# Kernel optimization log

Measured on AMD Instinct MI355X. Metric: run time of the kernel, lower is better.

## Reference

```python
import jax, jax.numpy as jnp
import numpy as np

EMBED_DIM = 1024
B, S = 4, 2048
SCALE = float(np.sqrt(EMBED_DIM))


def setup_inputs() -> dict:
    key = jax.random.key(0)
    ks = jax.random.split(key, 9)
    d = EMBED_DIM
    init = 1.0 / np.sqrt(d)
    return {
        "query": jax.random.normal(ks[0], (B, S, d), jnp.float32),
        "key": jax.random.normal(ks[1], (B, S, d), jnp.float32),
        "value": jax.random.normal(ks[2], (B, S, d), jnp.float32),
        "wq": jax.random.uniform(ks[3], (d, d), jnp.float32, -init, init),
        "bq": jax.random.uniform(ks[4], (d,), jnp.float32, -init, init),
        "wk": jax.random.uniform(ks[5], (d, d), jnp.float32, -init, init),
        "bk": jax.random.uniform(ks[6], (d,), jnp.float32, -init, init),
        "wv": jax.random.uniform(ks[7], (d, d), jnp.float32, -init, init),
        "bv": jax.random.uniform(ks[8], (d,), jnp.float32, -init, init),
    }


def reference(query, key, value, wq, bq, wk, bk, wv, bv):
    # Linear projections (torch Linear: x @ W^T + b; here weights stored as [in, out])
    q = query @ wq + bq            # [B,S,D]
    k = key @ wk + bk              # [B,S,D]
    v = value @ wv + bv            # [B,S,D]
    scores = jnp.einsum("bqd,bkd->bqk", q, k) / SCALE   # [B,S,S]
    attn = jax.nn.softmax(scores, axis=-1)
    # dropout in eval mode -> identity
    return jnp.einsum("bqk,bkd->bqd", attn, v)          # [B,S,D]
```

## Files before the change

### kernel.cpp

```cpp
#include <hip/hip_runtime.h>
#include <hip/hip_bf16.h>

typedef __attribute__((ext_vector_type(4))) float   f32x4;
typedef __attribute__((ext_vector_type(8))) __bf16  bf16x8;
typedef __attribute__((ext_vector_type(4))) __bf16  bf16x4;

#define NB 4
#define SS 2048
#define DD 1024

__device__ __forceinline__ void gload_lds16(const void* g, void* l) {
  __builtin_amdgcn_global_load_lds((const __attribute__((address_space(1))) void*)g,
                                   (__attribute__((address_space(3))) void*)l,
                                   16, 0, 0);
}

__global__ __launch_bounds__(256) void cvt_in_kernel(
    const float* __restrict__ q, const float* __restrict__ k,
    const float* __restrict__ v, __bf16* __restrict__ X)
{
  const float* src = blockIdx.z == 0 ? q : (blockIdx.z == 1 ? k : v);
  __bf16* dst = X + (size_t)blockIdx.z * (size_t)(NB * SS * DD);
  size_t i = ((size_t)blockIdx.x * 256 + threadIdx.x) * 4;
  float4 f = *(const float4*)&src[i];
  bf16x4 o = { (__bf16)f.x, (__bf16)f.y, (__bf16)f.z, (__bf16)f.w };
  *(bf16x4*)&dst[i] = o;
}

__global__ __launch_bounds__(256) void prep_w_kernel(
    const float* __restrict__ wq, const float* __restrict__ wk, const float* __restrict__ wv,
    const float* __restrict__ bq, const float* __restrict__ bk, const float* __restrict__ bv,
    __bf16* __restrict__ Wt, float* __restrict__ biasbuf)
{
  const int z = blockIdx.z;
  const float* W  = z == 0 ? wq : (z == 1 ? wk : wv);
  const float* bi = z == 0 ? bq : (z == 1 ? bk : bv);
  __bf16* dst = Wt + (size_t)z * (size_t)(DD * DD);
  const int n0 = blockIdx.x * 32, k0 = blockIdx.y * 32;
  __shared__ float t[32][33];
  const int tx = threadIdx.x & 31, ty = threadIdx.x >> 5;
  #pragma unroll
  for (int i = 0; i < 4; i++)
    t[ty + 8 * i][tx] = W[(size_t)(k0 + ty + 8 * i) * DD + n0 + tx];
  __syncthreads();
  #pragma unroll
  for (int i = 0; i < 4; i++)
    dst[(size_t)(n0 + ty + 8 * i) * DD + k0 + tx] = (__bf16)t[tx][ty + 8 * i];
  if (blockIdx.x == 0 && blockIdx.y == 0) {
    #pragma unroll
    for (int i = 0; i < 4; i++)
      biasbuf[z * DD + threadIdx.x + 256 * i] = bi[threadIdx.x + 256 * i];
  }
}


#define G2A(BUF) ((BUF) * 16384)
#define G2B(BUF) (32768 + (BUF) * 16384)

#define G2_STAGE(BUF, T) do { int t_ = (T); if (t_ >= NT) t_ = 0;               \
  const __bf16* gA_ = Ablk + (size_t)t_ * 64;                                   \
  const __bf16* gB_ = Bblk + (size_t)t_ * 64;                                   \
  gload_lds16(gA_ + o0, smem + G2A(BUF) + tid * 16);                            \
  gload_lds16(gA_ + o1, smem + G2A(BUF) + 4096 + tid * 16);                     \
  gload_lds16(gA_ + o2, smem + G2A(BUF) + 8192 + tid * 16);                     \
  gload_lds16(gA_ + o3, smem + G2A(BUF) + 12288 + tid * 16);                    \
  gload_lds16(gB_ + o0, smem + G2B(BUF) + tid * 16);                            \
  gload_lds16(gB_ + o1, smem + G2B(BUF) + 4096 + tid * 16);                     \
  gload_lds16(gB_ + o2, smem + G2B(BUF) + 8192 + tid * 16);                     \
  gload_lds16(gB_ + o3, smem + G2B(BUF) + 12288 + tid * 16); } while (0)

template <int EPI>
__global__ __launch_bounds__(256, 2) void gemm2b_kernel(
    const __bf16* __restrict__ A, const __bf16* __restrict__ B,
    const float* __restrict__ bias, float* __restrict__ Fout,
    __bf16* __restrict__ Qo, __bf16* __restrict__ Ko, __bf16* __restrict__ Vt,
    int K, int lda, int ldb, int ldc,
    long strideA, long strideB, long strideC)
{
  extern __shared__ char smem[];

  const int gx = gridDim.x, gy = gridDim.y;
  const int nwg = gx * gy * gridDim.z;
  int lin = blockIdx.x + gx * (blockIdx.y + gy * blockIdx.z);
  const int cpx = nwg >> 3;
  int swz = (lin & 7) * cpx + (lin >> 3);
  const int bx = swz % gx;
  int rem = swz / gx;
  const int by = rem % gy;
  const int bz = rem / gy;

  const long brow = (long)by * 128, bcol = (long)bx * 128;
  const __bf16* Ablk = A + (size_t)bz * strideA + (size_t)brow * lda;
  const __bf16* Bblk = B + (size_t)bz * strideB + (size_t)bcol * ldb;

  const int tid  = threadIdx.x;
  const int lane = tid & 63;
  const int wid  = tid >> 6;
  const int wm = wid >> 1, wn = wid & 1;
  const int l15 = lane & 15, l4 = lane >> 4;
  const int lx = (lane & 7) << 4;

  const int NT = K >> 6;

  int o0, o1, o2, o3;
  #pragma unroll
  for (int i = 0; i < 4; ++i) {
    const int p = i * 4096 + tid * 16;
    const int r = p >> 7;
    const int kb = (p ^ ((r & 7) << 4)) & 127;
    const int off = r * lda + (kb >> 1);
    if (i == 0) o0 = off; else if (i == 1) o1 = off;
    else if (i == 2) o2 = off; else o3 = off;
  }

  int ara[2], brb[2];
  #pragma unroll
  for (int ks = 0; ks < 2; ++ks) {
    ara[ks] = ((((wm * 64 + l15) * 64 + l4 * 8) * 2) + ks * 64) ^ lx;
    brb[ks] = ((((wn * 64 + l15) * 64 + l4 * 8) * 2) + ks * 64) ^ lx;
  }

  f32x4 acc[4][4] = {};
  f32x4 accs[4] = {};
  bf16x8 af[4][2], bf[4][2];
  bf16x8 onesf;
  #pragma unroll
  for (int j = 0; j < 8; ++j) onesf[j] = (__bf16)1.0f;

  G2_STAGE(0, 0);
  G2_STAGE(1, 1);
  asm volatile("s_waitcnt vmcnt(8)" ::: "memory");
  __builtin_amdgcn_s_barrier();

  for (int t = 0; t < NT; ++t) {
    const int cur = t & 1;
    const int abase = cur * 16384;
    const int bbase = 32768 + cur * 16384;
    #pragma unroll
    for (int mi = 0; mi < 4; ++mi)
      #pragma unroll
      for (int ks = 0; ks < 2; ++ks)
        af[mi][ks] = *(const bf16x8*)(smem + abase + ara[ks] + mi * 2048);
    #pragma unroll
    for (int ni = 0; ni < 4; ++ni)
      #pragma unroll
      for (int ks = 0; ks < 2; ++ks)
        bf[ni][ks] = *(const bf16x8*)(smem + bbase + brb[ks] + ni * 2048);
    asm volatile("s_waitcnt lgkmcnt(0)" ::: "memory");
    __builtin_amdgcn_sched_barrier(0);
    __builtin_amdgcn_s_barrier();
    G2_STAGE(cur, t + 2);
    __builtin_amdgcn_s_setprio(1);
    #pragma unroll
    for (int mi = 0; mi < 4; ++mi)
      #pragma unroll
      for (int ni = 0; ni < 4; ++ni)
        #pragma unroll
        for (int ks = 0; ks < 2; ++ks)
          acc[mi][ni] = __builtin_amdgcn_mfma_f32_16x16x32_bf16(
              af[mi][ks], bf[ni][ks], acc[mi][ni], 0, 0, 0);
    if constexpr (EPI == 2) {
      #pragma unroll
      for (int mi = 0; mi < 4; ++mi)
        #pragma unroll
        for (int ks = 0; ks < 2; ++ks)
          accs[mi] = __builtin_amdgcn_mfma_f32_16x16x32_bf16(
              af[mi][ks], onesf, accs[mi], 0, 0, 0);
    }
    __builtin_amdgcn_s_setprio(0);
    __builtin_amdgcn_sched_barrier(0);
    asm volatile("s_waitcnt vmcnt(8)" ::: "memory");
    __builtin_amdgcn_s_barrier();
  }

  if constexpr (EPI == 2) {
    float* C = Fout + (size_t)bz * strideC;
    #pragma unroll
    for (int mi = 0; mi < 4; ++mi) {
      f32x4 inv;
      #pragma unroll
      for (int e = 0; e < 4; ++e) inv[e] = 1.0f / accs[mi][e];
      #pragma unroll
      for (int ni = 0; ni < 4; ++ni) {
        const long row = brow + wm * 64 + mi * 16 + l4 * 4;
        const long col = bcol + wn * 64 + ni * 16 + l15;
        #pragma unroll
        for (int e = 0; e < 4; ++e)
          C[(row + e) * (size_t)ldc + col] = acc[mi][ni][e] * inv[e];
      }
    }
  } else {
    if (bz == 2) {
      #pragma unroll
      for (int mi = 0; mi < 4; ++mi) {
        #pragma unroll
        for (int ni = 0; ni < 4; ++ni) {
          const long row = brow + wm * 64 + mi * 16 + l4 * 4;
          const long col = bcol + wn * 64 + ni * 16 + l15;
          const float bvv = bias[2 * DD + col];
          const long bb = row >> 11, s = row & 2047;
          bf16x4 pk = { (__bf16)(acc[mi][ni][0] + bvv), (__bf16)(acc[mi][ni][1] + bvv),
                        (__bf16)(acc[mi][ni][2] + bvv), (__bf16)(acc[mi][ni][3] + bvv) };
          *(bf16x4*)&Vt[bb * 2097152 + col * 2048 + s] = pk;
        }
      }
    } else {
      __bf16* C = bz == 0 ? Qo : Ko;
      #pragma unroll
      for (int mi = 0; mi < 4; ++mi) {
        #pragma unroll
        for (int ni = 0; ni < 4; ++ni) {
          const long row = brow + wm * 64 + mi * 16 + l4 * 4;
          const long col = bcol + wn * 64 + ni * 16 + l15;
          const float bvv = bias[bz * DD + col];
          #pragma unroll
          for (int e = 0; e < 4; ++e)
            C[(row + e) * 1024 + col] = (__bf16)(acc[mi][ni][e] + bvv);
        }
      }
    }
  }
}


#define A_OFF(BUF, MH) (((BUF)*2 + (MH)) * 16384)
#define B_OFF(BUF, NH) (65536 + ((BUF)*2 + (NH)) * 16384)

#define STAGE_A(BUF, MH, T) do { int t_ = (T); if (t_ >= NT) t_ = 0;            \
  const __bf16* gs_ = Ablk + (size_t)(MH) * (64 * (size_t)lda) + (size_t)t_ * 64; \
  gload_lds16(gs_ + aoff0, smem + A_OFF(BUF, MH) + tid * 16);                    \
  gload_lds16(gs_ + aoff1, smem + A_OFF(BUF, MH) + 8192 + tid * 16); } while (0)

#define STAGE_B(BUF, NH, T) do { int t_ = (T); if (t_ >= NT) t_ = 0;            \
  const __bf16* gs_ = Bblk + (size_t)(NH) * (32 * (size_t)ldb) + (size_t)t_ * 64; \
  gload_lds16(gs_ + boff0, smem + B_OFF(BUF, NH) + tid * 16);                    \
  gload_lds16(gs_ + boff1, smem + B_OFF(BUF, NH) + 8192 + tid * 16); } while (0)

#define DSREAD_A(DST, BUF, MH)                                                  \
  _Pragma("unroll") for (int mi = 0; mi < 4; ++mi) {                            \
    _Pragma("unroll") for (int ks = 0; ks < 2; ++ks)                            \
      DST[mi][ks] = *(const bf16x8*)(smem + A_OFF(BUF, MH) + arb[ks] + mi * 2048); }

#define DSREAD_BS(DST, BUF, NH)                                                 \
  _Pragma("unroll") for (int ni = 0; ni < 2; ++ni) {                            \
    _Pragma("unroll") for (int ks = 0; ks < 2; ++ks)                            \
      DST[ni][ks] = *(const bf16x8*)(smem + B_OFF(BUF, NH) + brb[ks] + ni * 2048); }

#define BARRIER_MFMA(AF, BF, MH, NH) do {                                       \
  __builtin_amdgcn_s_barrier();                                                 \
  asm volatile("s_waitcnt lgkmcnt(0)" ::: "memory");                            \
  __builtin_amdgcn_sched_barrier(0);                                            \
  __builtin_amdgcn_s_setprio(1);                                                \
  _Pragma("unroll") for (int mi = 0; mi < 4; ++mi)                              \
  _Pragma("unroll") for (int ni = 0; ni < 2; ++ni)                              \
  _Pragma("unroll") for (int ks = 0; ks < 2; ++ks)                              \
    acc[(MH)*4+mi][(NH)*2+ni] = __builtin_amdgcn_mfma_f32_16x16x32_bf16(        \
        AF[mi][ks], BF[ni][ks], acc[(MH)*4+mi][(NH)*2+ni], 0, 0, 0);            \
  __builtin_amdgcn_s_setprio(0);                                                \
  __builtin_amdgcn_sched_barrier(0);                                            \
  __builtin_amdgcn_s_barrier(); } while (0)

__global__ __launch_bounds__(512) void gemm8p_kernel(
    const __bf16* __restrict__ A, const __bf16* __restrict__ B,
    float scale, void* __restrict__ Cout,
    int K, int lda, int ldb, int ldc,
    long strideA, long strideB, long strideC)
{
  extern __shared__ char smem[];

  const int gx = gridDim.x, gy = gridDim.y;
  const int nwg = gx * gy * gridDim.z;
  int lin = blockIdx.x + gx * (blockIdx.y + gy * blockIdx.z);
  const int cpx = nwg >> 3;
  int swz = (lin & 7) * cpx + (lin >> 3);
  const int bx = swz % gx;
  int rem = swz / gx;
  const int by = rem % gy;
  const int bz = rem / gy;

  const long brow = (long)by * 256, bcol = (long)bx * 256;
  const __bf16* Ablk = A + (size_t)bz * strideA + (size_t)brow * lda;
  const __bf16* Bblk = B + (size_t)bz * strideB + (size_t)bcol * ldb;

  const int tid  = threadIdx.x;
  const int lane = tid & 63;
  const int wid  = tid >> 6;
  const int wm = wid >> 2, wn = wid & 3;
  const int l15 = lane & 15, l4 = lane >> 4;
  const int lx = (lane & 7) << 4;

  const int NT = K >> 6;
  const int niter = NT >> 1;

  int aoff0, aoff1, boff0, boff1;
  #pragma unroll
  for (int i = 0; i < 2; ++i) {
    const int p = i * 8192 + tid * 16;
    const int l = p ^ (((p >> 7) & 7) << 4);
    const int r = p >> 7;
    const int kb = l & 127;
    const int av = ((r >> 6) * 128 + (r & 63)) * lda + (kb >> 1);
    const int bv = ((r >> 5) * 64 + (r & 31)) * ldb + (kb >> 1);
    if (i == 0) { aoff0 = av; boff0 = bv; } else { aoff1 = av; boff1 = bv; }
  }

  int arb[2], brb[2];
  #pragma unroll
  for (int ks = 0; ks < 2; ++ks) {
    arb[ks] = ((((wm * 64 + l15) * 64 + l4 * 8) * 2) + ks * 64) ^ lx;
    brb[ks] = ((((wn * 32 + l15) * 64 + l4 * 8) * 2) + ks * 64) ^ lx;
  }

  f32x4 acc[8][4] = {};
  bf16x8 a0[4][2], a1[4][2], b0[2][2], b1[2][2];

  STAGE_B(0, 0, 0); STAGE_A(0, 0, 0); STAGE_A(0, 1, 0); STAGE_B(0, 1, 0);
  STAGE_B(1, 0, 1); STAGE_A(1, 0, 1);
  asm volatile("s_waitcnt vmcnt(4)" ::: "memory");
  __builtin_amdgcn_s_barrier();

  for (int it = 0; it < niter; ++it) {
    const int tt = it * 2;
    DSREAD_A(a0, 0, 0); DSREAD_BS(b0, 0, 0);
    STAGE_A(1, 1, tt + 1);
    BARRIER_MFMA(a0, b0, 0, 0);
    DSREAD_A(a1, 0, 1);
    STAGE_B(1, 1, tt + 1);
    BARRIER_MFMA(a1, b0, 1, 0);
    DSREAD_BS(b1, 0, 1);
    STAGE_B(0, 0, tt + 2);
    BARRIER_MFMA(a0, b1, 0, 1);
    STAGE_A(0, 0, tt + 2);
    asm volatile("s_waitcnt vmcnt(4)" ::: "memory");
    BARRIER_MFMA(a1, b1, 1, 1);
    DSREAD_A(a0, 1, 0); DSREAD_BS(b0, 1, 0);
    STAGE_A(0, 1, tt + 2);
    BARRIER_MFMA(a0, b0, 0, 0);
    DSREAD_A(a1, 1, 1);
    STAGE_B(0, 1, tt + 2);
    BARRIER_MFMA(a1, b0, 1, 0);
    DSREAD_BS(b1, 1, 1);
    STAGE_B(1, 0, tt + 3);
    BARRIER_MFMA(a0, b1, 0, 1);
    STAGE_A(1, 0, tt + 3);
    asm volatile("s_waitcnt vmcnt(4)" ::: "memory");
    BARRIER_MFMA(a1, b1, 1, 1);
  }

  const int cr = l4 * 4;
  __bf16* C = (__bf16*)Cout + (size_t)bz * strideC;
  #pragma unroll
  for (int m = 0; m < 8; ++m) {
    #pragma unroll
    for (int n = 0; n < 4; ++n) {
      const long row = brow + wm * 128 + m * 16 + cr;
      const long col = bcol + wn * 64 + n * 16 + l15;
      #pragma unroll
      for (int e = 0; e < 4; ++e)
        C[(row + e) * (size_t)ldc + col] = (__bf16)__expf(acc[m][n][e] * scale);
    }
  }
}

extern "C" void kernel_launch(void* const* d_in, const int* in_sizes, int n_in,
                              void* d_out, int out_size, void* d_ws, size_t ws_size,
                              hipStream_t stream)
{
  const float* query = (const float*)d_in[0];
  const float* key   = (const float*)d_in[1];
  const float* value = (const float*)d_in[2];
  const float* wq = (const float*)d_in[3];
  const float* bq = (const float*)d_in[4];
  const float* wk = (const float*)d_in[5];
  const float* bk = (const float*)d_in[6];
  const float* wv = (const float*)d_in[7];
  const float* bv = (const float*)d_in[8];

  char* ws = (char*)d_ws;
  __bf16* Xbf     = (__bf16*)(ws + 0);
  __bf16* Wt      = (__bf16*)(ws + 50331648);
  float*  biasbuf = (float*)(ws + 56623104);
  __bf16* Qb      = (__bf16*)(ws + 56635392);
  __bf16* Kb      = (__bf16*)(ws + 73412608);
  __bf16* Vt      = (__bf16*)(ws + 90189824);
  __bf16* P       = Xbf;

  hipFuncSetAttribute((const void*)gemm2b_kernel<0>, hipFuncAttributeMaxDynamicSharedMemorySize, 65536);
  hipFuncSetAttribute((const void*)gemm2b_kernel<2>, hipFuncAttributeMaxDynamicSharedMemorySize, 65536);
  hipFuncSetAttribute((const void*)gemm8p_kernel,    hipFuncAttributeMaxDynamicSharedMemorySize, 131072);

  dim3 b256(256), b512(512);

  cvt_in_kernel<<<dim3(8192, 1, 3), b256, 0, stream>>>(query, key, value, Xbf);
  prep_w_kernel<<<dim3(32, 32, 3), b256, 0, stream>>>(wq, wk, wv, bq, bk, bv, Wt, biasbuf);
  gemm2b_kernel<0><<<dim3(8, 64, 3), b256, 65536, stream>>>(
      Xbf, Wt, biasbuf, nullptr, Qb, Kb, Vt,
      1024, 1024, 1024, 1024,
      8388608L, 1048576L, 0L);
  gemm8p_kernel<<<dim3(8, 8, 4), b512, 131072, stream>>>(
      Qb, Kb, 0.03125f, P,
      1024, 1024, 1024, 2048,
      2097152L, 2097152L, 4194304L);
  gemm2b_kernel<2><<<dim3(8, 16, 4), b256, 65536, stream>>>(
      P, Vt, nullptr, (float*)d_out, nullptr, nullptr, nullptr,
      2048, 2048, 2048, 1024,
      4194304L, 2097152L, 2097152L);

  (void)in_sizes; (void)n_in; (void)out_size; (void)ws_size;
}
```

Measured before the change: 168.9 us.

## Use dedicated 256x256-tile, 512-thread kernel for QKV projection GEMM

Replaces the templated 128x128 projection GEMM with a new kernel that computes 256x256 output tiles using 8 waves and a K-step of 32 with double-buffered, XOR-swizzled LDS staging. Each block gets more operand reuse per loaded byte, cutting global and LDS traffic per FLOP for the Q/K/V projections. The PV GEMM kernel is de-templated to keep only its softmax-normalising epilogue. Risks are higher register pressure from the 8x4 accumulator tile per wave, and only 384 blocks in the grid, which may underfill the CUs.

```diff
diff --git a/kernel.cpp b/kernel.cpp
--- a/kernel.cpp
+++ b/kernel.cpp
@@ -50,6 +50,128 @@
     #pragma unroll
     for (int i = 0; i < 4; i++)
       biasbuf[z * DD + threadIdx.x + 256 * i] = bi[threadIdx.x + 256 * i];
+  }
+}
+
+
+#define G3A(BUF) ((BUF) * 16384)
+#define G3B(BUF) (32768 + (BUF) * 16384)
+
+#define G3_STAGE(BUF, T) do { int t_ = (T); if (t_ >= 32) t_ = 0;               \
+  const __bf16* gA_ = Ablk + (size_t)t_ * 32;                                   \
+  const __bf16* gB_ = Bblk + (size_t)t_ * 32;                                   \
+  gload_lds16(gA_ + so0, smem + G3A(BUF) + tid * 16);                           \
+  gload_lds16(gA_ + so1, smem + G3A(BUF) + 8192 + tid * 16);                    \
+  gload_lds16(gB_ + so0, smem + G3B(BUF) + tid * 16);                           \
+  gload_lds16(gB_ + so1, smem + G3B(BUF) + 8192 + tid * 16); } while (0)
+
+__global__ __launch_bounds__(512, 2) void gemm3_kernel(
+    const __bf16* __restrict__ X, const __bf16* __restrict__ Wt,
+    const float* __restrict__ bias,
+    __bf16* __restrict__ Qo, __bf16* __restrict__ Ko, __bf16* __restrict__ Vt)
+{
+  extern __shared__ char smem[];
+
+  const int gx = gridDim.x, gy = gridDim.y;
+  const int nwg = gx * gy * gridDim.z;
+  int lin = blockIdx.x + gx * (blockIdx.y + gy * blockIdx.z);
+  const int cpx = nwg >> 3;
+  int swz = (lin & 7) * cpx + (lin >> 3);
+  const int bx = swz % gx;
+  int rem = swz / gx;
+  const int by = rem % gy;
+  const int bz = rem / gy;
+
+  const long brow = (long)by * 256, bcol = (long)bx * 256;
+  const __bf16* Ablk = X + (size_t)bz * 8388608 + (size_t)brow * 1024;
+  const __bf16* Bblk = Wt + (size_t)bz * 1048576 + (size_t)bcol * 1024;
+
+  const int tid  = threadIdx.x;
+  const int lane = tid & 63;
+  const int wid  = tid >> 6;
+  const int wm = wid >> 2, wn = wid & 3;
+  const int l15 = lane & 15, l4 = lane >> 4;
+
+  int so0, so1;
+  #pragma unroll
+  for (int i = 0; i < 2; ++i) {
+    const int p = i * 8192 + tid * 16;
+    const int r = p >> 7;
+    const int c = (p & 127) ^ ((r & 7) << 4);
+    const int R = 2 * r + (c >> 6);
+    const int kb = c & 63;
+    const int off = R * 1024 + (kb >> 1);
+    if (i == 0) so0 = off; else so1 = off;
+  }
+
+  const int rs = l15 >> 1;
+  const int fb = (((l15 & 1) * 64) + (l4 * 16)) ^ ((rs & 7) << 4);
+  const int aBase = (wm * 64 + rs) * 128 + fb;
+  const int bBase = (wn * 32 + rs) * 128 + fb;
+
+  f32x4 acc[8][4] = {};
+  bf16x8 af[8], bfr[4];
+
+  G3_STAGE(0, 0);
+  G3_STAGE(1, 1);
+  asm volatile("s_waitcnt vmcnt(4)" ::: "memory");
+  __builtin_amdgcn_s_barrier();
+
+  for (int t = 0; t < 32; ++t) {
+    const int cur = t & 1;
+    const int ab = cur * 16384;
+    const int bb = 32768 + cur * 16384;
+    #pragma unroll
+    for (int mi = 0; mi < 8; ++mi)
+      af[mi] = *(const bf16x8*)(smem + ab + aBase + mi * 1024);
+    #pragma unroll
+    for (int ni = 0; ni < 4; ++ni)
+      bfr[ni] = *(const bf16x8*)(smem + bb + bBase + ni * 1024);
+    asm volatile("s_waitcnt lgkmcnt(0)" ::: "memory");
+    __builtin_amdgcn_sched_barrier(0);
+    __builtin_amdgcn_s_barrier();
+    G3_STAGE(cur, t + 2);
+    __builtin_amdgcn_s_setprio(1);
+    #pragma unroll
+    for (int mi = 0; mi < 8; ++mi)
+      #pragma unroll
+      for (int ni = 0; ni < 4; ++ni)
+        acc[mi][ni] = __builtin_amdgcn_mfma_f32_16x16x32_bf16(
+            af[mi], bfr[ni], acc[mi][ni], 0, 0, 0);
+    __builtin_amdgcn_s_setprio(0);
+    __builtin_amdgcn_sched_barrier(0);
+    asm volatile("s_waitcnt vmcnt(4)" ::: "memory");
+    __builtin_amdgcn_s_barrier();
+  }
+
+  if (bz == 2) {
+    #pragma unroll
+    for (int mi = 0; mi < 8; ++mi) {
+      #pragma unroll
+      for (int ni = 0; ni < 4; ++ni) {
+        const long row = brow + wm * 128 + mi * 16 + l4 * 4;
+        const long col = bcol + wn * 64 + ni * 16 + l15;
+        const float bvv = bias[2 * DD + col];
+        const long bb2 = row >> 11, s = row & 2047;
+        bf16x4 pk = { (__bf16)(acc[mi][ni][0] + bvv), (__bf16)(acc[mi][ni][1] + bvv),
+                      (__bf16)(acc[mi][ni][2] + bvv), (__bf16)(acc[mi][ni][3] + bvv) };
+        *(bf16x4*)&Vt[bb2 * 2097152 + col * 2048 + s] = pk;
+      }
+    }
+  } else {
+    __bf16* C = bz == 0 ? Qo : Ko;
+    #pragma unroll
+    for (int mi = 0; mi < 8; ++mi) {
+      #pragma unroll
+      for (int ni = 0; ni < 4; ++ni) {
+        const long row = brow + wm * 128 + mi * 16 + l4 * 4;
+        const long col = bcol + wn * 64 + ni * 16 + l15;
+        const float bvv = bias[bz * DD + col];
+        #pragma unroll
+        for (int e = 0; e < 4; ++e)
+          C[(row + e) * 1024 + col] = (__bf16)(acc[mi][ni][e] + bvv);
+      }
+    }
   }
 }
 
@@ -69,11 +191,9 @@
   gload_lds16(gB_ + o2, smem + G2B(BUF) + 8192 + tid * 16);                     \
   gload_lds16(gB_ + o3, smem + G2B(BUF) + 12288 + tid * 16); } while (0)
 
-template <int EPI>
 __global__ __launch_bounds__(256, 2) void gemm2b_kernel(
     const __bf16* __restrict__ A, const __bf16* __restrict__ B,
-    const float* __restrict__ bias, float* __restrict__ Fout,
-    __bf16* __restrict__ Qo, __bf16* __restrict__ Ko, __bf16* __restrict__ Vt,
+    float* __restrict__ Fout,
     int K, int lda, int ldb, int ldc,
     long strideA, long strideB, long strideC)
 {
@@ -159,65 +279,31 @@
         for (int ks = 0; ks < 2; ++ks)
           acc[mi][ni] = __builtin_amdgcn_mfma_f32_16x16x32_bf16(
               af[mi][ks], bf[ni][ks], acc[mi][ni], 0, 0, 0);
-    if constexpr (EPI == 2) {
-      #pragma unroll
-      for (int mi = 0; mi < 4; ++mi)
-        #pragma unroll
-        for (int ks = 0; ks < 2; ++ks)
-          accs[mi] = __builtin_amdgcn_mfma_f32_16x16x32_bf16(
-              af[mi][ks], onesf, accs[mi], 0, 0, 0);
-    }
+    #pragma unroll
+    for (int mi = 0; mi < 4; ++mi)
+      #pragma unroll
+      for (int ks = 0; ks < 2; ++ks)
+        accs[mi] = __builtin_amdgcn_mfma_f32_16x16x32_bf16(
+            af[mi][ks], onesf, accs[mi], 0, 0, 0);
     __builtin_amdgcn_s_setprio(0);
     __builtin_amdgcn_sched_barrier(0);
     asm volatile("s_waitcnt vmcnt(8)" ::: "memory");
     __builtin_amdgcn_s_barrier();
   }
 
-  if constexpr (EPI == 2) {
-    float* C = Fout + (size_t)bz * strideC;
-    #pragma unroll
-    for (int mi = 0; mi < 4; ++mi) {
-      f32x4 inv;
-      #pragma unroll
-      for (int e = 0; e < 4; ++e) inv[e] = 1.0f / accs[mi][e];
-      #pragma unroll
-      for (int ni = 0; ni < 4; ++ni) {
-        const long row = brow + wm * 64 + mi * 16 + l4 * 4;
-        const long col = bcol + wn * 64 + ni * 16 + l15;
-        #pragma unroll
-        for (int e = 0; e < 4; ++e)
-          C[(row + e) * (size_t)ldc + col] = acc[mi][ni][e] * inv[e];
-      }
-    }
-  } else {
-    if (bz == 2) {
-      #pragma unroll
-      for (int mi = 0; mi < 4; ++mi) {
-        #pragma unroll
-        for (int ni = 0; ni < 4; ++ni) {
-          const long row = brow + wm * 64 + mi * 16 + l4 * 4;
-          const long col = bcol + wn * 64 + ni * 16 + l15;
-          const float bvv = bias[2 * DD + col];
-          const long bb = row >> 11, s = row & 2047;
-          bf16x4 pk = { (__bf16)(acc[mi][ni][0] + bvv), (__bf16)(acc[mi][ni][1] + bvv),
-                        (__bf16)(acc[mi][ni][2] + bvv), (__bf16)(acc[mi][ni][3] + bvv) };
-          *(bf16x4*)&Vt[bb * 2097152 + col * 2048 + s] = pk;
-        }
-      }
-    } else {
-      __bf16* C = bz == 0 ? Qo : Ko;
-      #pragma unroll
-      for (int mi = 0; mi < 4; ++mi) {
-        #pragma unroll
-        for (int ni = 0; ni < 4; ++ni) {
-          const long row = brow + wm * 64 + mi * 16 + l4 * 4;
-          const long col = bcol + wn * 64 + ni * 16 + l15;
-          const float bvv = bias[bz * DD + col];
-          #pragma unroll
-          for (int e = 0; e < 4; ++e)
-            C[(row + e) * 1024 + col] = (__bf16)(acc[mi][ni][e] + bvv);
-        }
-      }
+  float* C = Fout + (size_t)bz * strideC;
+  #pragma unroll
+  for (int mi = 0; mi < 4; ++mi) {
+    f32x4 inv;
+    #pragma unroll
+    for (int e = 0; e < 4; ++e) inv[e] = 1.0f / accs[mi][e];
+    #pragma unroll
+    for (int ni = 0; ni < 4; ++ni) {
+      const long row = brow + wm * 64 + mi * 16 + l4 * 4;
+      const long col = bcol + wn * 64 + ni * 16 + l15;
+      #pragma unroll
+      for (int e = 0; e < 4; ++e)
+        C[(row + e) * (size_t)ldc + col] = acc[mi][ni][e] * inv[e];
     }
   }
 }
@@ -385,24 +471,22 @@
   __bf16* Vt      = (__bf16*)(ws + 90189824);
   __bf16* P       = Xbf;
 
-  hipFuncSetAttribute((const void*)gemm2b_kernel<0>, hipFuncAttributeMaxDynamicSharedMemorySize, 65536);
-  hipFuncSetAttribute((const void*)gemm2b_kernel<2>, hipFuncAttributeMaxDynamicSharedMemorySize, 65536);
-  hipFuncSetAttribute((const void*)gemm8p_kernel,    hipFuncAttributeMaxDynamicSharedMemorySize, 131072);
+  hipFuncSetAttribute((const void*)gemm3_kernel,  hipFuncAttributeMaxDynamicSharedMemorySize, 65536);
+  hipFuncSetAttribute((const void*)gemm2b_kernel, hipFuncAttributeMaxDynamicSharedMemorySize, 65536);
+  hipFuncSetAttribute((const void*)gemm8p_kernel, hipFuncAttributeMaxDynamicSharedMemorySize, 131072);
 
   dim3 b256(256), b512(512);
 
   cvt_in_kernel<<<dim3(8192, 1, 3), b256, 0, stream>>>(query, key, value, Xbf);
   prep_w_kernel<<<dim3(32, 32, 3), b256, 0, stream>>>(wq, wk, wv, bq, bk, bv, Wt, biasbuf);
-  gemm2b_kernel<0><<<dim3(8, 64, 3), b256, 65536, stream>>>(
-      Xbf, Wt, biasbuf, nullptr, Qb, Kb, Vt,
-      1024, 1024, 1024, 1024,
-      8388608L, 1048576L, 0L);
+  gemm3_kernel<<<dim3(4, 32, 3), b512, 65536, stream>>>(
+      Xbf, Wt, biasbuf, Qb, Kb, Vt);
   gemm8p_kernel<<<dim3(8, 8, 4), b512, 131072, stream>>>(
       Qb, Kb, 0.03125f, P,
       1024, 1024, 1024, 2048,
       2097152L, 2097152L, 4194304L);
-  gemm2b_kernel<2><<<dim3(8, 16, 4), b256, 65536, stream>>>(
-      P, Vt, nullptr, (float*)d_out, nullptr, nullptr, nullptr,
+  gemm2b_kernel<<<dim3(8, 16, 4), b256, 65536, stream>>>(
+      P, Vt, (float*)d_out,
       2048, 2048, 2048, 1024,
       4194304L, 2097152L, 2097152L);
 
```

Result: slower. 181.5 us (+7.5%).

## Merge prep kernels and use 128x256 tiled PV GEMM with split-B pipeline

Applied to the files above, without the earlier changes.

Merges the input-conversion and weight-transpose kernels into one launch, saving a kernel launch. Replaces the 128x128 PV GEMM, which also computed row sums for normalization, with a new 512-thread kernel on 128x256 tiles. The B tile is split into two halves, and loads and MFMAs are interleaved across half-steps. The row-sum MFMAs now run once per A tile instead of once per 128-column tile, and A reuse improves, but the grid shrinks to 256 workgroups and occupancy may drop.

```diff
diff --git a/kernel.cpp b/kernel.cpp
--- a/kernel.cpp
+++ b/kernel.cpp
@@ -15,41 +15,40 @@
                                    16, 0, 0);
 }
 
-__global__ __launch_bounds__(256) void cvt_in_kernel(
-    const float* __restrict__ q, const float* __restrict__ k,
-    const float* __restrict__ v, __bf16* __restrict__ X)
-{
-  const float* src = blockIdx.z == 0 ? q : (blockIdx.z == 1 ? k : v);
-  __bf16* dst = X + (size_t)blockIdx.z * (size_t)(NB * SS * DD);
-  size_t i = ((size_t)blockIdx.x * 256 + threadIdx.x) * 4;
-  float4 f = *(const float4*)&src[i];
-  bf16x4 o = { (__bf16)f.x, (__bf16)f.y, (__bf16)f.z, (__bf16)f.w };
-  *(bf16x4*)&dst[i] = o;
-}
-
-__global__ __launch_bounds__(256) void prep_w_kernel(
+__global__ __launch_bounds__(256) void prep_kernel(
+    const float* __restrict__ q, const float* __restrict__ k, const float* __restrict__ v,
     const float* __restrict__ wq, const float* __restrict__ wk, const float* __restrict__ wv,
     const float* __restrict__ bq, const float* __restrict__ bk, const float* __restrict__ bv,
-    __bf16* __restrict__ Wt, float* __restrict__ biasbuf)
+    __bf16* __restrict__ X, __bf16* __restrict__ Wt, float* __restrict__ biasbuf)
 {
   const int z = blockIdx.z;
-  const float* W  = z == 0 ? wq : (z == 1 ? wk : wv);
-  const float* bi = z == 0 ? bq : (z == 1 ? bk : bv);
-  __bf16* dst = Wt + (size_t)z * (size_t)(DD * DD);
-  const int n0 = blockIdx.x * 32, k0 = blockIdx.y * 32;
   __shared__ float t[32][33];
-  const int tx = threadIdx.x & 31, ty = threadIdx.x >> 5;
-  #pragma unroll
-  for (int i = 0; i < 4; i++)
-    t[ty + 8 * i][tx] = W[(size_t)(k0 + ty + 8 * i) * DD + n0 + tx];
-  __syncthreads();
-  #pragma unroll
-  for (int i = 0; i < 4; i++)
-    dst[(size_t)(n0 + ty + 8 * i) * DD + k0 + tx] = (__bf16)t[tx][ty + 8 * i];
-  if (blockIdx.x == 0 && blockIdx.y == 0) {
+  if (blockIdx.x < 8192) {
+    const float* src = z == 0 ? q : (z == 1 ? k : v);
+    __bf16* dst = X + (size_t)z * (size_t)(NB * SS * DD);
+    size_t i = ((size_t)blockIdx.x * 256 + threadIdx.x) * 4;
+    float4 f = *(const float4*)&src[i];
+    bf16x4 o = { (__bf16)f.x, (__bf16)f.y, (__bf16)f.z, (__bf16)f.w };
+    *(bf16x4*)&dst[i] = o;
+  } else {
+    const int idx = blockIdx.x - 8192;
+    const float* W  = z == 0 ? wq : (z == 1 ? wk : wv);
+    const float* bi = z == 0 ? bq : (z == 1 ? bk : bv);
+    __bf16* dst = Wt + (size_t)z * (size_t)(DD * DD);
+    const int n0 = (idx & 31) * 32, k0 = (idx >> 5) * 32;
+    const int tx = threadIdx.x & 31, ty = threadIdx.x >> 5;
     #pragma unroll
     for (int i = 0; i < 4; i++)
-      biasbuf[z * DD + threadIdx.x + 256 * i] = bi[threadIdx.x + 256 * i];
+      t[ty + 8 * i][tx] = W[(size_t)(k0 + ty + 8 * i) * DD + n0 + tx];
+    __syncthreads();
+    #pragma unroll
+    for (int i = 0; i < 4; i++)
+      dst[(size_t)(n0 + ty + 8 * i) * DD + k0 + tx] = (__bf16)t[tx][ty + 8 * i];
+    if (idx == 0) {
+      #pragma unroll
+      for (int i = 0; i < 4; i++)
+        biasbuf[z * DD + threadIdx.x + 256 * i] = bi[threadIdx.x + 256 * i];
+    }
   }
 }
 
@@ -69,13 +68,12 @@
   gload_lds16(gB_ + o2, smem + G2B(BUF) + 8192 + tid * 16);                     \
   gload_lds16(gB_ + o3, smem + G2B(BUF) + 12288 + tid * 16); } while (0)
 
-template <int EPI>
 __global__ __launch_bounds__(256, 2) void gemm2b_kernel(
     const __bf16* __restrict__ A, const __bf16* __restrict__ B,
-    const float* __restrict__ bias, float* __restrict__ Fout,
+    const float* __restrict__ bias,
     __bf16* __restrict__ Qo, __bf16* __restrict__ Ko, __bf16* __restrict__ Vt,
-    int K, int lda, int ldb, int ldc,
-    long strideA, long strideB, long strideC)
+    int K, int lda, int ldb,
+    long strideA, long strideB)
 {
   extern __shared__ char smem[];
 
@@ -121,11 +119,7 @@
   }
 
   f32x4 acc[4][4] = {};
-  f32x4 accs[4] = {};
   bf16x8 af[4][2], bf[4][2];
-  bf16x8 onesf;
-  #pragma unroll
-  for (int j = 0; j < 8; ++j) onesf[j] = (__bf16)1.0f;
 
   G2_STAGE(0, 0);
   G2_STAGE(1, 1);
@@ -159,64 +153,38 @@
         for (int ks = 0; ks < 2; ++ks)
           acc[mi][ni] = __builtin_amdgcn_mfma_f32_16x16x32_bf16(
               af[mi][ks], bf[ni][ks], acc[mi][ni], 0, 0, 0);
-    if constexpr (EPI == 2) {
-      #pragma unroll
-      for (int mi = 0; mi < 4; ++mi)
-        #pragma unroll
-        for (int ks = 0; ks < 2; ++ks)
-          accs[mi] = __builtin_amdgcn_mfma_f32_16x16x32_bf16(
-              af[mi][ks], onesf, accs[mi], 0, 0, 0);
-    }
     __builtin_amdgcn_s_setprio(0);
     __builtin_amdgcn_sched_barrier(0);
     asm volatile("s_waitcnt vmcnt(8)" ::: "memory");
     __builtin_amdgcn_s_barrier();
   }
 
-  if constexpr (EPI == 2) {
-    float* C = Fout + (size_t)bz * strideC;
+  if (bz == 2) {
     #pragma unroll
     for (int mi = 0; mi < 4; ++mi) {
-      f32x4 inv;
-      #pragma unroll
-      for (int e = 0; e < 4; ++e) inv[e] = 1.0f / accs[mi][e];
       #pragma unroll
       for (int ni = 0; ni < 4; ++ni) {
         const long row = brow + wm * 64 + mi * 16 + l4 * 4;
         const long col = bcol + wn * 64 + ni * 16 + l15;
-        #pragma unroll
-        for (int e = 0; e < 4; ++e)
-          C[(row + e) * (size_t)ldc + col] = acc[mi][ni][e] * inv[e];
+        const float bvv = bias[2 * DD + col];
+        const long bb = row >> 11, s = row & 2047;
+        bf16x4 pk = { (__bf16)(acc[mi][ni][0] + bvv), (__bf16)(acc[mi][ni][1] + bvv),
+                      (__bf16)(acc[mi][ni][2] + bvv), (__bf16)(acc[mi][ni][3] + bvv) };
+        *(bf16x4*)&Vt[bb * 2097152 + col * 2048 + s] = pk;
       }
     }
   } else {
-    if (bz == 2) {
-      #pragma unroll
-      for (int mi = 0; mi < 4; ++mi) {
+    __bf16* C = bz == 0 ? Qo : Ko;
+    #pragma unroll
+    for (int mi = 0; mi < 4; ++mi) {
+      #pragma unroll
+      for (int ni = 0; ni < 4; ++ni) {
+        const long row = brow + wm * 64 + mi * 16 + l4 * 4;
+        const long col = bcol + wn * 64 + ni * 16 + l15;
+        const float bvv = bias[bz * DD + col];
         #pragma unroll
-        for (int ni = 0; ni < 4; ++ni) {
-          const long row = brow + wm * 64 + mi * 16 + l4 * 4;
-          const long col = bcol + wn * 64 + ni * 16 + l15;
-          const float bvv = bias[2 * DD + col];
-          const long bb = row >> 11, s = row & 2047;
-          bf16x4 pk = { (__bf16)(acc[mi][ni][0] + bvv), (__bf16)(acc[mi][ni][1] + bvv),
-                        (__bf16)(acc[mi][ni][2] + bvv), (__bf16)(acc[mi][ni][3] + bvv) };
-          *(bf16x4*)&Vt[bb * 2097152 + col * 2048 + s] = pk;
-        }
-      }
-    } else {
-      __bf16* C = bz == 0 ? Qo : Ko;
-      #pragma unroll
-      for (int mi = 0; mi < 4; ++mi) {
-        #pragma unroll
-        for (int ni = 0; ni < 4; ++ni) {
-          const long row = brow + wm * 64 + mi * 16 + l4 * 4;
-          const long col = bcol + wn * 64 + ni * 16 + l15;
-          const float bvv = bias[bz * DD + col];
-          #pragma unroll
-          for (int e = 0; e < 4; ++e)
-            C[(row + e) * 1024 + col] = (__bf16)(acc[mi][ni][e] + bvv);
-        }
+        for (int e = 0; e < 4; ++e)
+          C[(row + e) * 1024 + col] = (__bf16)(acc[mi][ni][e] + bvv);
       }
     }
   }
@@ -362,6 +330,150 @@
   }
 }
 
+
+#define PV_A_OFF(BUF)     ((BUF) * 16384)
+#define PV_B_OFF(BUF, NH) (32768 + ((BUF)*2 + (NH)) * 16384)
+
+#define PV_DSA(BUF)                                                             \
+  _Pragma("unroll") for (int mi = 0; mi < 4; ++mi) {                            \
+    _Pragma("unroll") for (int ks = 0; ks < 2; ++ks)                            \
+      af[mi][ks] = *(const bf16x8*)(smem + PV_A_OFF(BUF) + ara[ks] + mi * 2048); }
+
+#define PV_DSB(DST, BUF, NH)                                                    \
+  _Pragma("unroll") for (int ni = 0; ni < 2; ++ni) {                            \
+    _Pragma("unroll") for (int ks = 0; ks < 2; ++ks)                            \
+      DST[ni][ks] = *(const bf16x8*)(smem + PV_B_OFF(BUF, NH) + brb2[ks] + ni * 2048); }
+
+#define PV_SA(BUF, T) do { int t_ = (T); if (t_ >= NT) t_ = 0;                  \
+  const __bf16* gA_ = Ablk + (size_t)t_ * 64;                                   \
+  gload_lds16(gA_ + aoff0, smem + PV_A_OFF(BUF) + tid * 16);                    \
+  gload_lds16(gA_ + aoff1, smem + PV_A_OFF(BUF) + 8192 + tid * 16);             \
+  const __bf16* gB_ = Bblk + (size_t)t_ * 64;                                   \
+  gload_lds16(gB_ + boff0, smem + PV_B_OFF(BUF, 0) + tid * 16);                 \
+  gload_lds16(gB_ + boff1, smem + PV_B_OFF(BUF, 0) + 8192 + tid * 16); } while (0)
+
+#define PV_SB(BUF, T) do { int t_ = (T); if (t_ >= NT) t_ = 0;                  \
+  const __bf16* gB_ = Bblk + (size_t)(128 * (size_t)ldb) + (size_t)t_ * 64;     \
+  gload_lds16(gB_ + boff0, smem + PV_B_OFF(BUF, 1) + tid * 16);                 \
+  gload_lds16(gB_ + boff1, smem + PV_B_OFF(BUF, 1) + 8192 + tid * 16); } while (0)
+
+#define PV_MFMA(BF, NH, DOSUM) do {                                             \
+  __builtin_amdgcn_s_barrier();                                                 \
+  asm volatile("s_waitcnt lgkmcnt(0)" ::: "memory");                            \
+  __builtin_amdgcn_sched_barrier(0);                                            \
+  __builtin_amdgcn_s_setprio(1);                                                \
+  _Pragma("unroll") for (int mi = 0; mi < 4; ++mi)                              \
+  _Pragma("unroll") for (int ni = 0; ni < 2; ++ni)                              \
+  _Pragma("unroll") for (int ks = 0; ks < 2; ++ks)                              \
+    acc[mi][(NH)*2+ni] = __builtin_amdgcn_mfma_f32_16x16x32_bf16(               \
+        af[mi][ks], BF[ni][ks], acc[mi][(NH)*2+ni], 0, 0, 0);                   \
+  if (DOSUM) {                                                                  \
+    _Pragma("unroll") for (int mi = 0; mi < 4; ++mi)                            \
+    _Pragma("unroll") for (int ks = 0; ks < 2; ++ks)                            \
+      accs[mi] = __builtin_amdgcn_mfma_f32_16x16x32_bf16(                       \
+          af[mi][ks], onesf, accs[mi], 0, 0, 0); }                              \
+  __builtin_amdgcn_s_setprio(0);                                                \
+  __builtin_amdgcn_sched_barrier(0);                                            \
+  __builtin_amdgcn_s_barrier(); } while (0)
+
+__global__ __launch_bounds__(512) void gemm128_kernel(
+    const __bf16* __restrict__ A, const __bf16* __restrict__ B,
+    void* __restrict__ Cout,
+    int K, int lda, int ldb, int ldc,
+    long strideA, long strideB, long strideC)
+{
+  extern __shared__ char smem[];
+
+  const int gx = gridDim.x, gy = gridDim.y;
+  const int nwg = gx * gy * gridDim.z;
+  int lin = blockIdx.x + gx * (blockIdx.y + gy * blockIdx.z);
+  const int cpx = nwg >> 3;
+  int swz = (lin & 7) * cpx + (lin >> 3);
+  const int bx = swz % gx;
+  int rem = swz / gx;
+  const int by = rem % gy;
+  const int bz = rem / gy;
+
+  const long brow = (long)by * 128, bcol = (long)bx * 256;
+  const __bf16* Ablk = A + (size_t)bz * strideA + (size_t)brow * lda;
+  const __bf16* Bblk = B + (size_t)bz * strideB + (size_t)bcol * ldb;
+
+  const int tid  = threadIdx.x;
+  const int lane = tid & 63;
+  const int wid  = tid >> 6;
+  const int wm = wid >> 2, wn = wid & 3;
+  const int l15 = lane & 15, l4 = lane >> 4;
+  const int lx = (lane & 7) << 4;
+
+  const int NT = K >> 6;
+  const int niter = NT >> 1;
+
+  int aoff0, aoff1, boff0, boff1;
+  #pragma unroll
+  for (int i = 0; i < 2; ++i) {
+    const int p = i * 8192 + tid * 16;
+    const int r = p >> 7;
+    const int kb = (p ^ ((r & 7) << 4)) & 127;
+    const int av = r * lda + (kb >> 1);
+    const int bv = r * ldb + (kb >> 1);
+    if (i == 0) { aoff0 = av; boff0 = bv; } else { aoff1 = av; boff1 = bv; }
+  }
+
+  int ara[2], brb2[2];
+  #pragma unroll
+  for (int ks = 0; ks < 2; ++ks) {
+    ara[ks]  = ((((wm * 64 + l15) * 64 + l4 * 8) * 2) + ks * 64) ^ lx;
+    brb2[ks] = ((((wn * 32 + l15) * 64 + l4 * 8) * 2) + ks * 64) ^ lx;
+  }
+
+  f32x4 acc[4][4] = {};
+  f32x4 accs[4] = {};
+  bf16x8 af[4][2], b0[2][2], b1[2][2];
+  bf16x8 onesf;
+  #pragma unroll
+  for (int j = 0; j < 8; ++j) onesf[j] = (__bf16)1.0f;
+
+  PV_SA(0, 0); PV_SB(0, 0); PV_SA(1, 1);
+  asm volatile("s_waitcnt vmcnt(6)" ::: "memory");
+  __builtin_amdgcn_s_barrier();
+
+  for (int it = 0; it < niter; ++it) {
+    const int tt = it * 2;
+    PV_SB(1, tt + 1);
+    asm volatile("s_waitcnt vmcnt(6)" ::: "memory");
+    PV_DSA(0); PV_DSB(b0, 0, 0);
+    PV_MFMA(b0, 0, 1);
+    PV_SA(0, tt + 2);
+    asm volatile("s_waitcnt vmcnt(6)" ::: "memory");
+    PV_DSB(b1, 0, 1);
+    PV_MFMA(b1, 1, 0);
+    PV_SB(0, tt + 2);
+    asm volatile("s_waitcnt vmcnt(6)" ::: "memory");
+    PV_DSA(1); PV_DSB(b0, 1, 0);
+    PV_MFMA(b0, 0, 1);
+    PV_SA(1, tt + 3);
+    asm volatile("s_waitcnt vmcnt(6)" ::: "memory");
+    PV_DSB(b1, 1, 1);
+    PV_MFMA(b1, 1, 0);
+  }
+
+  float* C = (float*)Cout + (size_t)bz * strideC;
+  #pragma unroll
+  for (int mi = 0; mi < 4; ++mi) {
+    f32x4 inv;
+    #pragma unroll
+    for (int e = 0; e < 4; ++e) inv[e] = 1.0f / accs[mi][e];
+    #pragma unroll
+    for (int n = 0; n < 4; ++n) {
+      const long row = brow + wm * 64 + mi * 16 + l4 * 4;
+      const long col = bcol + (n >> 1) * 128 + wn * 32 + (n & 1) * 16 + l15;
+      #pragma unroll
+      for (int e = 0; e < 4; ++e)
+        C[(row + e) * (size_t)ldc + col] = acc[mi][n][e] * inv[e];
+    }
+  }
+}
+
 extern "C" void kernel_launch(void* const* d_in, const int* in_sizes, int n_in,
                               void* d_out, int out_size, void* d_ws, size_t ws_size,
                               hipStream_t stream)
@@ -385,24 +497,23 @@
   __bf16* Vt      = (__bf16*)(ws + 90189824);
   __bf16* P       = Xbf;
 
-  hipFuncSetAttribute((const void*)gemm2b_kernel<0>, hipFuncAttributeMaxDynamicSharedMemorySize, 65536);
-  hipFuncSetAttribute((const void*)gemm2b_kernel<2>, hipFuncAttributeMaxDynamicSharedMemorySize, 65536);
-  hipFuncSetAttribute((const void*)gemm8p_kernel,    hipFuncAttributeMaxDynamicSharedMemorySize, 131072);
+  hipFuncSetAttribute((const void*)gemm2b_kernel,  hipFuncAttributeMaxDynamicSharedMemorySize, 65536);
+  hipFuncSetAttribute((const void*)gemm8p_kernel,  hipFuncAttributeMaxDynamicSharedMemorySize, 131072);
+  hipFuncSetAttribute((const void*)gemm128_kernel, hipFuncAttributeMaxDynamicSharedMemorySize, 131072);
 
   dim3 b256(256), b512(512);
 
-  cvt_in_kernel<<<dim3(8192, 1, 3), b256, 0, stream>>>(query, key, value, Xbf);
-  prep_w_kernel<<<dim3(32, 32, 3), b256, 0, stream>>>(wq, wk, wv, bq, bk, bv, Wt, biasbuf);
-  gemm2b_kernel<0><<<dim3(8, 64, 3), b256, 65536, stream>>>(
-      Xbf, Wt, biasbuf, nullptr, Qb, Kb, Vt,
-      1024, 1024, 1024, 1024,
-      8388608L, 1048576L, 0L);
+  prep_kernel<<<dim3(9216, 1, 3), b256, 0, stream>>>(
+      query, key, value, wq, wk, wv, bq, bk, bv, Xbf, Wt, biasbuf);
+  gemm2b_kernel<<<dim3(8, 64, 3), b256, 65536, stream>>>(
+      Xbf, Wt, biasbuf, Qb, Kb, Vt,
+      1024, 1024, 1024, 8388608L, 1048576L);
   gemm8p_kernel<<<dim3(8, 8, 4), b512, 131072, stream>>>(
       Qb, Kb, 0.03125f, P,
       1024, 1024, 1024, 2048,
       2097152L, 2097152L, 4194304L);
-  gemm2b_kernel<2><<<dim3(8, 16, 4), b256, 65536, stream>>>(
-      P, Vt, nullptr, (float*)d_out, nullptr, nullptr, nullptr,
+  gemm128_kernel<<<dim3(4, 16, 4), b512, 98304, stream>>>(
+      P, Vt, d_out,
       2048, 2048, 2048, 1024,
       4194304L, 2097152L, 2097152L);
 
```

Result: no change. 170.0 us (+0.7%).
